# Performance work log

Hardware: AMD Instinct MI355X
Metric: run time of the kernel (lower is better)

## Reference

```python
import heapq
import jax, jax.numpy as jnp
import numpy as np

NB_CLASSES = 50257
INPUT_DIM = 512
BATCH = 1024
NB_REQ = 8


def build_huffman(nb_classes):
    """Replicates Huffmax.build: huffman tree over equal frequencies,
    codes padded with 0, paths padded with root node id."""
    heap = [(1, i, i) for i in range(nb_classes)]  # (freq, tiebreak, payload)
    heapq.heapify(heap)
    node_id = 0
    tiebreak = nb_classes
    while len(heap) > 1:
        f1, _, left = heapq.heappop(heap)
        f2, _, right = heapq.heappop(heap)
        heapq.heappush(heap, (f1 + f2, tiebreak, ('n', node_id, left, right)))
        node_id += 1
        tiebreak += 1
    root = heap[0][2]
    total_nodes = node_id  # = nb_classes - 1
    root_id = root[1]
    codes, paths = {}, {}
    stack = [(root, [], [])]
    while stack:
        node, code, path = stack.pop()
        if isinstance(node, tuple):
            _, nid, l, r = node
            stack.append((l, code + [0], path + [nid]))
            stack.append((r, code + [1], path + [nid]))
        else:
            codes[node] = code
            paths[node] = path
    max_depth = max(len(c) for c in codes.values())
    code_arr = np.zeros((nb_classes, max_depth), np.float32)
    path_arr = np.full((nb_classes, max_depth), root_id, np.int32)
    for c in range(nb_classes):
        code_arr[c, :len(codes[c])] = codes[c]
        path_arr[c, :len(paths[c])] = paths[c]
    return code_arr, path_arr, total_nodes


def setup_inputs() -> dict:
    key = jax.random.key(0)
    k1, k2, k3 = jax.random.split(key, 3)
    code_arr, path_arr, total_nodes = build_huffman(NB_CLASSES)
    input_vector = jax.random.normal(k1, (BATCH, INPUT_DIM), dtype=jnp.float32)
    target_classes = jax.random.randint(k2, (BATCH, NB_REQ), 0, NB_CLASSES, dtype=jnp.int32)
    # glorot-ish scaled node weights (original W is (total_nodes, input_dim, 1))
    W = jax.random.normal(k3, (total_nodes, INPUT_DIM), dtype=jnp.float32) * (1.0 / np.sqrt(INPUT_DIM))
    b = jnp.zeros((total_nodes,), dtype=jnp.float32)
    return {
        'input_vector': input_vector,
        'target_classes': target_classes,
        'W': W,
        'b': b,
        'class_paths': jnp.asarray(path_arr),
        'huffman_codes': jnp.asarray(code_arr),
    }


def reference(input_vector, target_classes, W, b, class_paths, huffman_codes):
    # req_nodes: (B, R, D) node ids along huffman path for each requested class
    req_nodes = class_paths[target_classes]
    # req_W: (B, R, D, I) gathered node weight rows; y = x . W_node + b_node
    req_W = W[req_nodes]
    y = jnp.einsum('bi,brdi->brd', input_vector, req_W) + b[req_nodes]
    y = jax.nn.sigmoid(y)
    codes = huffman_codes[target_classes]  # (B, R, D) in {0,1} (0-padded)
    # factor = y if code==0 else (1-y); product along the path
    return jnp.prod(codes + y - 2.0 * codes * y, axis=-1)
```

## Files before the change

### kernel.cpp

```cpp
#include <hip/hip_runtime.h>
#include <math.h>

#define WPB 4

template<int D>
__global__ __launch_bounds__(WPB * 64, 4)
void huff_kernel(const float* __restrict__ x,
                 const int*   __restrict__ tgt,
                 const float* __restrict__ W,
                 const float* __restrict__ bias,
                 const int*   __restrict__ paths,
                 const float* __restrict__ codes,
                 float*       __restrict__ out,
                 int R, int I, int npairs)
{
    const int lane = threadIdx.x & 63;
    const int wv   = threadIdx.x >> 6;
    const int p    = blockIdx.x * WPB + wv;
    if (p >= npairs) return;
    const int b = p / R;

    const float4* xrow = reinterpret_cast<const float4*>(x + (size_t)b * I);
    const float4 xa = xrow[lane];
    const float4 xb = xrow[lane + 64];

    const int c  = tgt[p];
    const int dd = (lane < D) ? lane : (D - 1);
    const int   nd = paths[(size_t)c * D + dd];
    const float cd = codes[(size_t)c * D + dd];
    const float bv = bias[nd];
    const float sd = 1.0f - 2.0f * cd;

    float acc[D];
    #pragma unroll
    for (int d = 0; d < D; ++d) {
        const int node = __shfl(nd, d, 64);
        const float4* wr = reinterpret_cast<const float4*>(W + (size_t)node * I);
        const float4 wa = wr[lane];
        const float4 wb = wr[lane + 64];
        acc[d] = xa.x * wa.x + xa.y * wa.y + xa.z * wa.z + xa.w * wa.w
               + xb.x * wb.x + xb.y * wb.y + xb.z * wb.z + xb.w * wb.w;
    }

    #pragma unroll
    for (int off = 32; off; off >>= 1) {
        #pragma unroll
        for (int d = 0; d < D; ++d)
            acc[d] += __shfl_xor(acc[d], off, 64);
    }

    float q = 1.0f;
    #pragma unroll
    for (int d = 0; d < D; ++d) {
        const float t = acc[d] + __shfl(bv, d, 64);
        const float s = __shfl(sd, d, 64);
        q *= 1.0f + __expf(-s * t);
    }
    if (lane == 0) out[p] = 1.0f / q;
}

__global__ __launch_bounds__(WPB * 64)
void huff_kernel_gen(const float* __restrict__ x, const int* __restrict__ tgt,
                     const float* __restrict__ W, const float* __restrict__ bias,
                     const int* __restrict__ paths, const float* __restrict__ codes,
                     float* __restrict__ out, int R, int I, int D, int npairs)
{
    const int lane = threadIdx.x & 63;
    const int p = blockIdx.x * WPB + (threadIdx.x >> 6);
    if (p >= npairs) return;
    const int b = p / R;
    const float4* xrow = reinterpret_cast<const float4*>(x + (size_t)b * I);
    const float4 xa = xrow[lane];
    const float4 xb = xrow[lane + 64];
    const int c = tgt[p];
    float q = 1.0f;
    for (int d = 0; d < D; ++d) {
        const int node = paths[(size_t)c * D + d];
        const float4* wr = reinterpret_cast<const float4*>(W + (size_t)node * I);
        const float4 wa = wr[lane];
        const float4 wb = wr[lane + 64];
        float acc = xa.x * wa.x + xa.y * wa.y + xa.z * wa.z + xa.w * wa.w
                  + xb.x * wb.x + xb.y * wb.y + xb.z * wb.z + xb.w * wb.w;
        #pragma unroll
        for (int off = 32; off; off >>= 1) acc += __shfl_xor(acc, off, 64);
        const float t = acc + bias[node];
        const float s = 1.0f - 2.0f * codes[(size_t)c * D + d];
        q *= 1.0f + __expf(-s * t);
    }
    if (lane == 0) out[p] = 1.0f / q;
}

extern "C" void kernel_launch(void* const* d_in, const int* in_sizes, int n_in,
                              void* d_out, int out_size, void* d_ws, size_t ws_size,
                              hipStream_t stream) {
    const float* x     = (const float*)d_in[0];
    const int*   tgt   = (const int*)  d_in[1];
    const float* W     = (const float*)d_in[2];
    const float* bias  = (const float*)d_in[3];
    const int*   paths = (const int*)  d_in[4];
    const float* codes = (const float*)d_in[5];
    float* out = (float*)d_out;

    const int N = in_sizes[3];
    const int C = N + 1;
    const int I = in_sizes[2] / N;
    const int B = in_sizes[0] / I;
    const int R = in_sizes[1] / B;
    const int D = in_sizes[4] / C;

    const int npairs = B * R;
    const int grid = (npairs + WPB - 1) / WPB;

    switch (D) {
    case 15: huff_kernel<15><<<grid, WPB * 64, 0, stream>>>(x, tgt, W, bias, paths, codes, out, R, I, npairs); break;
    case 16: huff_kernel<16><<<grid, WPB * 64, 0, stream>>>(x, tgt, W, bias, paths, codes, out, R, I, npairs); break;
    case 17: huff_kernel<17><<<grid, WPB * 64, 0, stream>>>(x, tgt, W, bias, paths, codes, out, R, I, npairs); break;
    case 18: huff_kernel<18><<<grid, WPB * 64, 0, stream>>>(x, tgt, W, bias, paths, codes, out, R, I, npairs); break;
    default: huff_kernel_gen<<<grid, WPB * 64, 0, stream>>>(x, tgt, W, bias, paths, codes, out, R, I, D, npairs); break;
    }
}
```

Baseline: 25.45 us.

## Stage gathered node weights through LDS with double-buffered async global loads

Replaces the per-pair wave kernel with a one-block-per-batch-row kernel. It loads x once into LDS and streams the 16 path-node weight rows for each of the 8 requested classes into a double-buffered LDS area using global_load_lds, overlapping the next pair's loads with the current dot products. Each of the 4 waves handles 4 depth levels, and the partial products are combined through shared memory. The new kernel hardcodes D=16, R=8, I=512, which fits the Huffman tree depth for 50257 classes, and the generic kernel stays as a fallback. This adds manual vmcnt bookkeeping and a large LDS footprint that may limit occupancy.

```diff
diff --git a/kernel.cpp b/kernel.cpp
--- a/kernel.cpp
+++ b/kernel.cpp
@@ -3,60 +3,106 @@
 
 #define WPB 4
 
-template<int D>
-__global__ __launch_bounds__(WPB * 64, 4)
-void huff_kernel(const float* __restrict__ x,
-                 const int*   __restrict__ tgt,
-                 const float* __restrict__ W,
-                 const float* __restrict__ bias,
-                 const int*   __restrict__ paths,
-                 const float* __restrict__ codes,
-                 float*       __restrict__ out,
-                 int R, int I, int npairs)
+__device__ __forceinline__ void gld16(const float* g, void* l) {
+    __builtin_amdgcn_global_load_lds((const __attribute__((address_space(1))) void*)g,
+                                     (__attribute__((address_space(3))) void*)l, 16, 0, 0);
+}
+
+__global__ __launch_bounds__(256)
+void huff_lds16(const float* __restrict__ x, const int* __restrict__ tgt,
+                const float* __restrict__ W, const float* __restrict__ bias,
+                const int* __restrict__ paths, const float* __restrict__ codes,
+                float* __restrict__ out)
 {
+    __shared__ float4 wbuf[2][16][128];
+    __shared__ float4 xbuf[128];
+    __shared__ float  qbuf[8][4];
+
     const int lane = threadIdx.x & 63;
-    const int wv   = threadIdx.x >> 6;
-    const int p    = blockIdx.x * WPB + wv;
-    if (p >= npairs) return;
-    const int b = p / R;
+    const int w    = threadIdx.x >> 6;
+    const int b    = blockIdx.x;
+    const int p0   = b * 8;
 
-    const float4* xrow = reinterpret_cast<const float4*>(x + (size_t)b * I);
-    const float4 xa = xrow[lane];
-    const float4 xb = xrow[lane + 64];
-
-    const int c  = tgt[p];
-    const int dd = (lane < D) ? lane : (D - 1);
-    const int   nd = paths[(size_t)c * D + dd];
-    const float cd = codes[(size_t)c * D + dd];
-    const float bv = bias[nd];
-    const float sd = 1.0f - 2.0f * cd;
-
-    float acc[D];
+    const int dd = lane & 15;
+    int nd[8]; float sd[8], bv[8];
     #pragma unroll
-    for (int d = 0; d < D; ++d) {
-        const int node = __shfl(nd, d, 64);
-        const float4* wr = reinterpret_cast<const float4*>(W + (size_t)node * I);
-        const float4 wa = wr[lane];
-        const float4 wb = wr[lane + 64];
-        acc[d] = xa.x * wa.x + xa.y * wa.y + xa.z * wa.z + xa.w * wa.w
-               + xb.x * wb.x + xb.y * wb.y + xb.z * wb.z + xb.w * wb.w;
+    for (int p = 0; p < 8; ++p) {
+        const int c = tgt[p0 + p];
+        nd[p] = paths[(size_t)c * 16 + dd];
+        const float cd = codes[(size_t)c * 16 + dd];
+        sd[p] = 1.0f - 2.0f * cd;
+        bv[p] = bias[nd[p]];
     }
 
+    asm volatile("s_waitcnt vmcnt(0)" ::: "memory");
+
+    if (w == 0) {
+        const float* xs = x + (size_t)b * 512 + lane * 4;
+        gld16(xs,       (float*)xbuf);
+        gld16(xs + 256, (float*)xbuf + 256);
+    }
     #pragma unroll
-    for (int off = 32; off; off >>= 1) {
+    for (int k = 0; k < 4; ++k) {
+        const int r = 4 * w + k;
+        const int node = __shfl(nd[0], r);
+        const float* src = W + (size_t)node * 512 + lane * 4;
+        gld16(src,       &wbuf[0][r][0]);
+        gld16(src + 256, (float*)&wbuf[0][r][0] + 256);
+    }
+    if (w == 0) { asm volatile("s_waitcnt vmcnt(8)" ::: "memory"); }
+    __builtin_amdgcn_s_barrier();
+    asm volatile("" ::: "memory");
+
+    const float4 xa = xbuf[lane];
+    const float4 xc = xbuf[lane + 64];
+
+    #pragma unroll
+    for (int t = 0; t < 8; ++t) {
+        if (t < 7) {
+            #pragma unroll
+            for (int k = 0; k < 4; ++k) {
+                const int r = 4 * w + k;
+                const int node = __shfl(nd[t + 1], r);
+                const float* src = W + (size_t)node * 512 + lane * 4;
+                gld16(src,       &wbuf[(t + 1) & 1][r][0]);
+                gld16(src + 256, (float*)&wbuf[(t + 1) & 1][r][0] + 256);
+            }
+            asm volatile("s_waitcnt vmcnt(8)" ::: "memory");
+        } else {
+            asm volatile("s_waitcnt vmcnt(0)" ::: "memory");
+        }
+
+        float acc[4];
         #pragma unroll
-        for (int d = 0; d < D; ++d)
-            acc[d] += __shfl_xor(acc[d], off, 64);
+        for (int k = 0; k < 4; ++k) {
+            const float4 wa = wbuf[t & 1][4 * w + k][lane];
+            const float4 wb = wbuf[t & 1][4 * w + k][lane + 64];
+            acc[k] = xa.x * wa.x + xa.y * wa.y + xa.z * wa.z + xa.w * wa.w
+                   + xc.x * wb.x + xc.y * wb.y + xc.z * wb.z + xc.w * wb.w;
+        }
+        #pragma unroll
+        for (int off = 32; off; off >>= 1) {
+            #pragma unroll
+            for (int k = 0; k < 4; ++k)
+                acc[k] += __shfl_xor(acc[k], off, 64);
+        }
+
+        float qw = 1.0f;
+        #pragma unroll
+        for (int k = 0; k < 4; ++k) {
+            const float tt = acc[k] + __shfl(bv[t], 4 * w + k);
+            const float s  = __shfl(sd[t], 4 * w + k);
+            qw *= 1.0f + __expf(-s * tt);
+        }
+        if (lane == 0) qbuf[t][w] = qw;
     }
 
-    float q = 1.0f;
-    #pragma unroll
-    for (int d = 0; d < D; ++d) {
-        const float t = acc[d] + __shfl(bv, d, 64);
-        const float s = __shfl(sd, d, 64);
-        q *= 1.0f + __expf(-s * t);
+    __syncthreads();
+    if (threadIdx.x < 8) {
+        const float q = qbuf[threadIdx.x][0] * qbuf[threadIdx.x][1]
+                      * qbuf[threadIdx.x][2] * qbuf[threadIdx.x][3];
+        out[p0 + threadIdx.x] = 1.0f / q;
     }
-    if (lane == 0) out[p] = 1.0f / q;
 }
 
 __global__ __launch_bounds__(WPB * 64)
@@ -109,13 +155,12 @@
     const int D = in_sizes[4] / C;
 
     const int npairs = B * R;
-    const int grid = (npairs + WPB - 1) / WPB;
 
-    switch (D) {
-    case 15: huff_kernel<15><<<grid, WPB * 64, 0, stream>>>(x, tgt, W, bias, paths, codes, out, R, I, npairs); break;
-    case 16: huff_kernel<16><<<grid, WPB * 64, 0, stream>>>(x, tgt, W, bias, paths, codes, out, R, I, npairs); break;
-    case 17: huff_kernel<17><<<grid, WPB * 64, 0, stream>>>(x, tgt, W, bias, paths, codes, out, R, I, npairs); break;
-    case 18: huff_kernel<18><<<grid, WPB * 64, 0, stream>>>(x, tgt, W, bias, paths, codes, out, R, I, npairs); break;
-    default: huff_kernel_gen<<<grid, WPB * 64, 0, stream>>>(x, tgt, W, bias, paths, codes, out, R, I, D, npairs); break;
+    if (D == 16 && R == 8 && I == 512) {
+        huff_lds16<<<B, 256, 0, stream>>>(x, tgt, W, bias, paths, codes, out);
+    } else {
+        const int grid = (npairs + WPB - 1) / WPB;
+        huff_kernel_gen<<<grid, WPB * 64, 0, stream>>>(x, tgt, W, bias, paths, codes,
+                                                       out, R, I, D, npairs);
     }
 }
```

Measured after the change: 33.09 us. 30.0% more time.
